# Kernel tuning notes

Hardware: AMD Instinct MI355X
Metric: run time of the kernel (lower is better)

The kernel has to match this reference:

```python
import jax, jax.numpy as jnp
import numpy as np

N, L, D_H, D_X = 512, 64, 256, 64
Q, N_TYP, N_TOK, N_MEM = 8192, 16, 32000, 262144
N_SEG = N * L


def setup_inputs() -> dict:
    key = jax.random.key(0)
    ks = jax.random.split(key, 16)
    inp = {}
    inp['h_grp'] = jax.random.normal(ks[0], (N, L, D_H), jnp.float32)
    inp['tok_emb'] = jax.random.normal(ks[1], (N_TOK, D_X), jnp.float32) * 0.02
    inp['Wq'] = jax.random.normal(ks[2], (D_H, 2 * D_H), jnp.float32) / np.sqrt(2 * D_H)
    inp['bq'] = jnp.zeros((D_H,), jnp.float32)
    inp['Wk'] = jax.random.normal(ks[3], (D_H, D_H), jnp.float32) / np.sqrt(D_H)
    inp['bk'] = jnp.zeros((D_H,), jnp.float32)
    inp['Wrel'] = jax.random.normal(ks[4], (N_TYP, 2 * D_H + D_X), jnp.float32) / np.sqrt(2 * D_H + D_X)
    inp['brel'] = jnp.zeros((N_TYP,), jnp.float32)
    inp['mem'] = jax.random.randint(ks[5], (N_MEM,), 0, N_TOK, jnp.int32)
    inp['grp'] = jax.random.randint(ks[6], (N_MEM,), 0, N_SEG, jnp.int32)
    inp['pos2grp'] = jax.random.randint(ks[7], (N, L), 0, N_SEG, jnp.int32)
    msk = jax.random.randint(ks[8], (N, L, 1), 0, 2, jnp.int32)
    inp['msk'] = msk.at[:, 0, :].set(1)  # ensure every group has a valid slot
    inp['idx'] = jnp.sort(jax.random.randint(ks[9], (Q,), 0, N, jnp.int32))
    inp['src'] = jax.random.randint(ks[10], (Q,), 0, L, jnp.int32)
    inp['dst'] = jax.random.randint(ks[11], (Q,), 0, L, jnp.int32)
    inp['typ'] = jax.random.randint(ks[12], (Q, N_TYP), 0, 2, jnp.int32)
    return inp


def reference(h_grp, tok_emb, Wq, bq, Wk, bk, Wrel, brel,
              mem, grp, pos2grp, msk, idx, src, dst, typ):
    n, l, d_h = h_grp.shape
    # x_grp = scatter_sum(tok_embedding(mem), grp, 0)[pos2grp]  -> (n, l, d_x)
    x_sum = jax.ops.segment_sum(tok_emb[mem], grp, num_segments=N_SEG)
    x_grp = x_sum[pos2grp]
    # q = cat([h_grp[idx, src], h_grp[idx, dst]], -1)  -> (Q, 2*d_h)
    q_in = jnp.concatenate([h_grp[idx, src], h_grp[idx, dst]], axis=-1)
    # attention(): per-query attention over its group's l positions
    qp = q_in @ Wq.T + bq                                # (Q, d_h)
    kp = h_grp @ Wk.T + bk                               # (n, l, d_h)
    s = jnp.einsum('qld,qd->ql', kp[idx], qp) / jnp.sqrt(jnp.float32(d_h))
    valid = msk[idx, :, 0].astype(bool)                  # (Q, l)
    s = jnp.where(valid, s, -jnp.inf)
    a = jax.nn.softmax(s, axis=1)                        # (Q, l)
    attn = jnp.einsum('ql,qld->qd', a, x_grp[idx])       # (Q, d_x)
    # rel head
    logit = jnp.concatenate([q_in, attn], axis=-1) @ Wrel.T + brel  # (Q, n_typ)
    # metrics
    gt = logit > 0
    eq = gt == (typ > 0)
    acc = eq.astype(jnp.float32).mean()
    em = jax.ops.segment_min(jnp.all(eq, axis=1).astype(jnp.int32), idx, num_segments=n)
    emr = em.astype(jnp.float32).mean()
    return logit, acc, emr, em
```

## Files before the change

kernel.cpp:

```cpp
#include <hip/hip_runtime.h>
#include <math.h>

#define N_    512
#define L_    64
#define DH    256
#define DX    64
#define Q_    8192
#define NTYP  16
#define NMEM  262144
#define NSEG  32768

typedef short bf16x8 __attribute__((ext_vector_type(8)));
typedef float f32x4  __attribute__((ext_vector_type(4)));

__device__ inline ushort f2bf(float x) {
    unsigned u = __float_as_uint(x);
    unsigned r = u + 0x7FFFu + ((u >> 16) & 1u);
    return (ushort)(r >> 16);
}

__global__ void k_init(int* __restrict__ em, int* __restrict__ eqcnt) {
    int t = blockIdx.x * blockDim.x + threadIdx.x;
    if (t < N_) em[t] = 0x7fffffff;
    if (t == 0) *eqcnt = 0;
}

__global__ __launch_bounds__(256) void k_hist(const int* __restrict__ grp,
                                              int* __restrict__ counts) {
    int e = blockIdx.x * 256 + threadIdx.x;
    atomicAdd(&counts[grp[e]], 1);
}

__global__ __launch_bounds__(1024) void k_scan(const int* __restrict__ counts,
                                               int* __restrict__ offsets,
                                               int* __restrict__ cursor) {
    __shared__ int ls[1024];
    int t = threadIdx.x;
    int c[32];
    int base = t * 32;
    int s = 0;
#pragma unroll
    for (int i = 0; i < 32; i++) { c[i] = counts[base + i]; s += c[i]; }
    ls[t] = s;
    __syncthreads();
    for (int off = 1; off < 1024; off <<= 1) {
        int v = (t >= off) ? ls[t - off] : 0;
        __syncthreads();
        ls[t] += v;
        __syncthreads();
    }
    int excl = (t == 0) ? 0 : ls[t - 1];
#pragma unroll
    for (int i = 0; i < 32; i++) {
        offsets[base + i] = excl;
        cursor[base + i] = excl;
        excl += c[i];
    }
}

__global__ __launch_bounds__(256) void k_bucket(const int* __restrict__ grp,
                                                const int* __restrict__ mem,
                                                int* __restrict__ cursor,
                                                int* __restrict__ sorted_mem) {
    int e = blockIdx.x * 256 + threadIdx.x;
    int g = grp[e];
    int pos = atomicAdd(&cursor[g], 1);
    sorted_mem[pos] = mem[e];
}

__global__ __launch_bounds__(256) void k_gsum(const float* __restrict__ tok,
                                              const int* __restrict__ sorted_mem,
                                              const int* __restrict__ offsets,
                                              const int* __restrict__ counts,
                                              float* __restrict__ xsum) {
    int g = blockIdx.x * 4 + (threadIdx.x >> 6);
    int lane = threadIdx.x & 63;
    int beg = offsets[g], cnt = counts[g];
    float acc = 0.f;
    for (int j = 0; j < cnt; j++) {
        int m = sorted_mem[beg + j];
        acc += tok[(size_t)m * 64 + lane];
    }
    xsum[(size_t)g * 64 + lane] = acc;
}

__global__ __launch_bounds__(256) void k_wcvt(const float* __restrict__ Wq,
                                              const float* __restrict__ Wk,
                                              const float* __restrict__ Wrel,
                                              ushort* __restrict__ Wqbf,
                                              ushort* __restrict__ WkTbf,
                                              ushort* __restrict__ Wrelbf) {
    int i = blockIdx.x * 256 + threadIdx.x;
    if (i < 131072) Wqbf[i] = f2bf(Wq[i]);
    if (i < 65536) {
        int kk = i >> 8, e = i & 255;
        WkTbf[e * 256 + kk] = f2bf(Wk[i]);
    }
    if (i < 9216) Wrelbf[i] = f2bf(Wrel[i]);
}

__global__ __launch_bounds__(256) void k_qin(const float* __restrict__ h,
                                             const int* __restrict__ idx,
                                             const int* __restrict__ src,
                                             const int* __restrict__ dst,
                                             ushort* __restrict__ qin) {
    int q = blockIdx.x * 2 + (threadIdx.x >> 7);
    int t = threadIdx.x & 127;
    int r = idx[q];
    int pos = (t < 64) ? src[q] : dst[q];
    float4 v = *(const float4*)(h + ((size_t)r * 64 + pos) * 256 + (t & 63) * 4);
    ushort4 o = { f2bf(v.x), f2bf(v.y), f2bf(v.z), f2bf(v.w) };
    *(ushort4*)(qin + (size_t)q * 512 + t * 4) = o;
}

__global__ __launch_bounds__(256) void k_gqp(const ushort* __restrict__ qin,
                                             const ushort* __restrict__ Wqbf,
                                             const float* __restrict__ bq,
                                             ushort* __restrict__ qp_bf) {
    int w = threadIdx.x >> 6, l = threadIdx.x & 63;
    int qb = (blockIdx.x >> 2) * 64 + (w >> 1) * 32;
    int db = (blockIdx.x & 3) * 64 + (w & 1) * 32;
    int lr = l & 15, lk = (l >> 4) * 8;
    f32x4 a00 = {0.f,0.f,0.f,0.f}, a01 = a00, a10 = a00, a11 = a00;
#pragma unroll 4
    for (int k0 = 0; k0 < 512; k0 += 32) {
        bf16x8 fa0 = *(const bf16x8*)(qin + (size_t)(qb + lr) * 512 + k0 + lk);
        bf16x8 fa1 = *(const bf16x8*)(qin + (size_t)(qb + 16 + lr) * 512 + k0 + lk);
        bf16x8 fb0 = *(const bf16x8*)(Wqbf + (size_t)(db + lr) * 512 + k0 + lk);
        bf16x8 fb1 = *(const bf16x8*)(Wqbf + (size_t)(db + 16 + lr) * 512 + k0 + lk);
        a00 = __builtin_amdgcn_mfma_f32_16x16x32_bf16(fa0, fb0, a00, 0, 0, 0);
        a01 = __builtin_amdgcn_mfma_f32_16x16x32_bf16(fa0, fb1, a01, 0, 0, 0);
        a10 = __builtin_amdgcn_mfma_f32_16x16x32_bf16(fa1, fb0, a10, 0, 0, 0);
        a11 = __builtin_amdgcn_mfma_f32_16x16x32_bf16(fa1, fb1, a11, 0, 0, 0);
    }
    int ocol = l & 15;
    float b0 = bq[db + ocol], b1 = bq[db + 16 + ocol];
#pragma unroll
    for (int r = 0; r < 4; r++) {
        int row = (l >> 4) * 4 + r;
        qp_bf[(size_t)(qb + row) * 256 + db + ocol]           = f2bf(a00[r] + b0);
        qp_bf[(size_t)(qb + row) * 256 + db + 16 + ocol]      = f2bf(a01[r] + b1);
        qp_bf[(size_t)(qb + 16 + row) * 256 + db + ocol]      = f2bf(a10[r] + b0);
        qp_bf[(size_t)(qb + 16 + row) * 256 + db + 16 + ocol] = f2bf(a11[r] + b1);
    }
}

__global__ __launch_bounds__(256) void k_gqk(const ushort* __restrict__ qp_bf,
                                             const ushort* __restrict__ WkTbf,
                                             float* __restrict__ qk) {
    int w = threadIdx.x >> 6, l = threadIdx.x & 63;
    int qb = (blockIdx.x >> 2) * 64 + (w >> 1) * 32;
    int eb = (blockIdx.x & 3) * 64 + (w & 1) * 32;
    int lr = l & 15, lk = (l >> 4) * 8;
    f32x4 a00 = {0.f,0.f,0.f,0.f}, a01 = a00, a10 = a00, a11 = a00;
#pragma unroll 4
    for (int k0 = 0; k0 < 256; k0 += 32) {
        bf16x8 fa0 = *(const bf16x8*)(qp_bf + (size_t)(qb + lr) * 256 + k0 + lk);
        bf16x8 fa1 = *(const bf16x8*)(qp_bf + (size_t)(qb + 16 + lr) * 256 + k0 + lk);
        bf16x8 fb0 = *(const bf16x8*)(WkTbf + (size_t)(eb + lr) * 256 + k0 + lk);
        bf16x8 fb1 = *(const bf16x8*)(WkTbf + (size_t)(eb + 16 + lr) * 256 + k0 + lk);
        a00 = __builtin_amdgcn_mfma_f32_16x16x32_bf16(fa0, fb0, a00, 0, 0, 0);
        a01 = __builtin_amdgcn_mfma_f32_16x16x32_bf16(fa0, fb1, a01, 0, 0, 0);
        a10 = __builtin_amdgcn_mfma_f32_16x16x32_bf16(fa1, fb0, a10, 0, 0, 0);
        a11 = __builtin_amdgcn_mfma_f32_16x16x32_bf16(fa1, fb1, a11, 0, 0, 0);
    }
    int ocol = l & 15;
#pragma unroll
    for (int r = 0; r < 4; r++) {
        int row = (l >> 4) * 4 + r;
        qk[(size_t)(qb + row) * 256 + eb + ocol]           = a00[r];
        qk[(size_t)(qb + row) * 256 + eb + 16 + ocol]      = a01[r];
        qk[(size_t)(qb + 16 + row) * 256 + eb + ocol]      = a10[r];
        qk[(size_t)(qb + 16 + row) * 256 + eb + 16 + ocol] = a11[r];
    }
}

__global__ __launch_bounds__(256) void k_htr(const float* __restrict__ h,
                                             float4* __restrict__ hT4) {
    __shared__ float hsT[256][65];
    int row = blockIdx.x;
    int t = threadIdx.x;
    const float4* h4 = (const float4*)(h + (size_t)row * 64 * 256);
    for (int i = t; i < 4096; i += 256) {
        int l = i >> 6, d4 = i & 63;
        float4 v = h4[i];
        hsT[d4 * 4 + 0][l] = v.x; hsT[d4 * 4 + 1][l] = v.y;
        hsT[d4 * 4 + 2][l] = v.z; hsT[d4 * 4 + 3][l] = v.w;
    }
    __syncthreads();
    float4* o4 = hT4 + (size_t)row * 4096;
    for (int i = t; i < 4096; i += 256) {
        int j4 = i >> 6, l = i & 63;
        float4 o = { hsT[4 * j4 + 0][l], hsT[4 * j4 + 1][l],
                     hsT[4 * j4 + 2][l], hsT[4 * j4 + 3][l] };
        o4[i] = o;
    }
}

__global__ __launch_bounds__(256) void k_attn4(const float4* __restrict__ hT4,
                                               const float* __restrict__ qk,
                                               const float* __restrict__ xsum,
                                               const int* __restrict__ pos2grp,
                                               const int* __restrict__ msk,
                                               const int* __restrict__ idx,
                                               ushort* __restrict__ attn_bf) {
    int wid  = threadIdx.x >> 6;
    int lane = threadIdx.x & 63;
    int bid = ((blockIdx.x & 7) << 8) | (blockIdx.x >> 3);
    int q = bid * 4 + wid;
    int row = idx[q];

    const float4* hT  = hT4 + (size_t)row * 4096;
    const float4* qk4 = (const float4*)(qk + (size_t)q * 256);
    float p = 0.f;
#pragma unroll 8
    for (int j4 = 0; j4 < 64; j4++) {
        float4 hv = hT[j4 * 64 + lane];
        float4 qv = qk4[j4];
        p = fmaf(hv.x, qv.x, fmaf(hv.y, qv.y,
            fmaf(hv.z, qv.z, fmaf(hv.w, qv.w, p))));
    }
    int v = msk[row * 64 + lane];
    float s = v ? p * 0.0625f : -INFINITY;

    float m = s;
#pragma unroll
    for (int off = 32; off; off >>= 1) m = fmaxf(m, __shfl_xor(m, off));
    float e = expf(s - m);
    float sum = e;
#pragma unroll
    for (int off = 32; off; off >>= 1) sum += __shfl_xor(sum, off);
    float a = e / sum;

    int g_l = pos2grp[row * 64 + lane];
    float acc = 0.f;
#pragma unroll 8
    for (int l = 0; l < 64; l++) {
        float al = __shfl(a, l);
        int g = __shfl(g_l, l);
        acc = fmaf(al, xsum[(size_t)g * 64 + lane], acc);
    }
    attn_bf[(size_t)q * 64 + lane] = f2bf(acc);
}

__global__ __launch_bounds__(256) void k_logit4(const ushort* __restrict__ qin,
                                                const ushort* __restrict__ attn_bf,
                                                const ushort* __restrict__ Wrelbf,
                                                const float* __restrict__ brel,
                                                const int* __restrict__ idx,
                                                const int* __restrict__ typ,
                                                float* __restrict__ out,
                                                int* __restrict__ em,
                                                int* __restrict__ eqcnt) {
    __shared__ int cnt;
    int w = threadIdx.x >> 6, l = threadIdx.x & 63;
    int qb = blockIdx.x * 64 + w * 16;
    int lr = l & 15, lk = (l >> 4) * 8;
    if (threadIdx.x == 0) cnt = 0;
    __syncthreads();

    f32x4 acc = {0.f, 0.f, 0.f, 0.f};
    const ushort* wrow = Wrelbf + lr * 576;
#pragma unroll 4
    for (int k0 = 0; k0 < 512; k0 += 32) {
        bf16x8 fa = *(const bf16x8*)(qin + (size_t)(qb + lr) * 512 + k0 + lk);
        bf16x8 fb = *(const bf16x8*)(wrow + k0 + lk);
        acc = __builtin_amdgcn_mfma_f32_16x16x32_bf16(fa, fb, acc, 0, 0, 0);
    }
#pragma unroll
    for (int k0 = 0; k0 < 64; k0 += 32) {
        bf16x8 fa = *(const bf16x8*)(attn_bf + (size_t)(qb + lr) * 64 + k0 + lk);
        bf16x8 fb = *(const bf16x8*)(wrow + 512 + k0 + lk);
        acc = __builtin_amdgcn_mfma_f32_16x16x32_bf16(fa, fb, acc, 0, 0, 0);
    }

    float b = brel[lr];
    int localcnt = 0;
#pragma unroll
    for (int r = 0; r < 4; r++) {
        int q = qb + (l >> 4) * 4 + r;
        float val = acc[r] + b;
        out[(size_t)q * 16 + lr] = val;
        int eq = ((val > 0.f) == (typ[q * 16 + lr] > 0)) ? 1 : 0;
        unsigned long long mask = __ballot(eq);
        if (lr == 0) {
            unsigned bits = (unsigned)((mask >> ((l >> 4) * 16)) & 0xFFFFull);
            localcnt += __popc(bits);
            int all = (bits == 0xFFFFu) ? 1 : 0;
            atomicMin(&em[idx[q]], all);
        }
    }
    if (lr == 0) atomicAdd(&cnt, localcnt);
    __syncthreads();
    if (threadIdx.x == 0) atomicAdd(eqcnt, cnt);
}

__global__ void k_fin(const int* __restrict__ em, const int* __restrict__ eqcnt,
                      float* __restrict__ out) {
    __shared__ float ssum[512];
    int t = threadIdx.x;
    int v = em[t];
    out[131074 + t] = (float)v;
    ssum[t] = (float)v;
    __syncthreads();
    for (int s = 256; s; s >>= 1) {
        if (t < s) ssum[t] += ssum[t + s];
        __syncthreads();
    }
    if (t == 0) {
        out[131073] = ssum[0] / 512.0f;
        out[131072] = (float)(*eqcnt) / (float)(Q_ * NTYP);
    }
}

extern "C" void kernel_launch(void* const* d_in, const int* in_sizes, int n_in,
                              void* d_out, int out_size, void* d_ws, size_t ws_size,
                              hipStream_t stream) {
    const float* h    = (const float*)d_in[0];
    const float* tok  = (const float*)d_in[1];
    const float* Wq   = (const float*)d_in[2];
    const float* bq   = (const float*)d_in[3];
    const float* Wk   = (const float*)d_in[4];
    const float* Wrel = (const float*)d_in[6];
    const float* brel = (const float*)d_in[7];
    const int* mem     = (const int*)d_in[8];
    const int* grp     = (const int*)d_in[9];
    const int* pos2grp = (const int*)d_in[10];
    const int* msk     = (const int*)d_in[11];
    const int* idx     = (const int*)d_in[12];
    const int* src     = (const int*)d_in[13];
    const int* dst     = (const int*)d_in[14];
    const int* typ     = (const int*)d_in[15];
    float* out = (float*)d_out;

    char* ws = (char*)d_ws;
    float* xsum    = (float*)ws;
    float* qk      = (float*)(ws + (size_t)( 8 << 20));
    ushort* qin    = (ushort*)(ws + (size_t)(16 << 20));
    ushort* qp_bf  = (ushort*)(ws + (size_t)(24 << 20));
    ushort* attn_bf= (ushort*)(ws + (size_t)(24 << 20));
    float4* hT4    = (float4*)(ws + (size_t)(28 << 20));
    int* counts     = (int*)(ws + (size_t)(60 << 20));
    int* offsets    = (int*)(ws + (size_t)(60 << 20) + (128 << 10));
    int* cursor     = (int*)(ws + (size_t)(60 << 20) + (256 << 10));
    int* sorted_mem = (int*)(ws + (size_t)(60 << 20) + (384 << 10));
    int* em         = (int*)(ws + (size_t)(61 << 20) + (512 << 10));
    int* eqcnt      = (int*)(ws + (size_t)(61 << 20) + (516 << 10));
    ushort* Wqbf    = (ushort*)(ws + (size_t)(61 << 20) + (520 << 10));
    ushort* WkTbf   = (ushort*)(ws + (size_t)(61 << 20) + (776 << 10));
    ushort* Wrelbf  = (ushort*)(ws + (size_t)(61 << 20) + (904 << 10));

    k_init<<<1, 512, 0, stream>>>(em, eqcnt);
    hipMemsetAsync(counts, 0, (size_t)NSEG * 4, stream);
    k_hist<<<NMEM / 256, 256, 0, stream>>>(grp, counts);
    k_scan<<<1, 1024, 0, stream>>>(counts, offsets, cursor);
    k_bucket<<<NMEM / 256, 256, 0, stream>>>(grp, mem, cursor, sorted_mem);
    k_gsum<<<NSEG / 4, 256, 0, stream>>>(tok, sorted_mem, offsets, counts, xsum);
    k_wcvt<<<512, 256, 0, stream>>>(Wq, Wk, Wrel, Wqbf, WkTbf, Wrelbf);
    k_qin<<<Q_ / 2, 256, 0, stream>>>(h, idx, src, dst, qin);
    k_gqp<<<(Q_ / 64) * 4, 256, 0, stream>>>(qin, Wqbf, bq, qp_bf);
    k_gqk<<<(Q_ / 64) * 4, 256, 0, stream>>>(qp_bf, WkTbf, qk);
    k_htr<<<N_, 256, 0, stream>>>(h, hT4);
    k_attn4<<<Q_ / 4, 256, 0, stream>>>(hT4, qk, xsum, pos2grp, msk, idx, attn_bf);
    k_logit4<<<Q_ / 64, 256, 0, stream>>>(qin, attn_bf, Wrelbf, brel, idx, typ, out, em, eqcnt);
    k_fin<<<1, 512, 0, stream>>>(em, eqcnt, out);
}
```

Baseline: 274.5 us.

## Fuse transpose into per-group MFMA attention kernel using sorted idx ranges

Replaces the h-transpose kernel and the per-query scalar attention kernel with one kernel per group row. Each block binary-searches the sorted idx for its query range, stages h and the gathered x_grp into shared memory as bf16, and computes scores and the attention-weighted sum with bf16 MFMA. qk is now written as bf16 instead of fp32. This removes one launch and the hT round trip, and reuses each group's h and x across all of its queries. In exchange, scores, probabilities and x lose precision, and load balance depends on how many queries land in each group.

```diff
diff --git a/kernel.cpp b/kernel.cpp
--- a/kernel.cpp
+++ b/kernel.cpp
@@ -147,7 +147,7 @@
 
 __global__ __launch_bounds__(256) void k_gqk(const ushort* __restrict__ qp_bf,
                                              const ushort* __restrict__ WkTbf,
-                                             float* __restrict__ qk) {
+                                             ushort* __restrict__ qk_bf) {
     int w = threadIdx.x >> 6, l = threadIdx.x & 63;
     int qb = (blockIdx.x >> 2) * 64 + (w >> 1) * 32;
     int eb = (blockIdx.x & 3) * 64 + (w & 1) * 32;
@@ -168,79 +168,139 @@
 #pragma unroll
     for (int r = 0; r < 4; r++) {
         int row = (l >> 4) * 4 + r;
-        qk[(size_t)(qb + row) * 256 + eb + ocol]           = a00[r];
-        qk[(size_t)(qb + row) * 256 + eb + 16 + ocol]      = a01[r];
-        qk[(size_t)(qb + 16 + row) * 256 + eb + ocol]      = a10[r];
-        qk[(size_t)(qb + 16 + row) * 256 + eb + 16 + ocol] = a11[r];
-    }
-}
-
-__global__ __launch_bounds__(256) void k_htr(const float* __restrict__ h,
-                                             float4* __restrict__ hT4) {
-    __shared__ float hsT[256][65];
-    int row = blockIdx.x;
-    int t = threadIdx.x;
-    const float4* h4 = (const float4*)(h + (size_t)row * 64 * 256);
-    for (int i = t; i < 4096; i += 256) {
-        int l = i >> 6, d4 = i & 63;
-        float4 v = h4[i];
-        hsT[d4 * 4 + 0][l] = v.x; hsT[d4 * 4 + 1][l] = v.y;
-        hsT[d4 * 4 + 2][l] = v.z; hsT[d4 * 4 + 3][l] = v.w;
-    }
-    __syncthreads();
-    float4* o4 = hT4 + (size_t)row * 4096;
-    for (int i = t; i < 4096; i += 256) {
-        int j4 = i >> 6, l = i & 63;
-        float4 o = { hsT[4 * j4 + 0][l], hsT[4 * j4 + 1][l],
-                     hsT[4 * j4 + 2][l], hsT[4 * j4 + 3][l] };
-        o4[i] = o;
-    }
-}
-
-__global__ __launch_bounds__(256) void k_attn4(const float4* __restrict__ hT4,
-                                               const float* __restrict__ qk,
+        qk_bf[(size_t)(qb + row) * 256 + eb + ocol]           = f2bf(a00[r]);
+        qk_bf[(size_t)(qb + row) * 256 + eb + 16 + ocol]      = f2bf(a01[r]);
+        qk_bf[(size_t)(qb + 16 + row) * 256 + eb + ocol]      = f2bf(a10[r]);
+        qk_bf[(size_t)(qb + 16 + row) * 256 + eb + 16 + ocol] = f2bf(a11[r]);
+    }
+}
+
+__global__ __launch_bounds__(256) void k_attn5(const float* __restrict__ h,
+                                               const ushort* __restrict__ qk_bf,
                                                const float* __restrict__ xsum,
                                                const int* __restrict__ pos2grp,
                                                const int* __restrict__ msk,
                                                const int* __restrict__ idx,
                                                ushort* __restrict__ attn_bf) {
-    int wid  = threadIdx.x >> 6;
-    int lane = threadIdx.x & 63;
-    int bid = ((blockIdx.x & 7) << 8) | (blockIdx.x >> 3);
-    int q = bid * 4 + wid;
-    int row = idx[q];
-
-    const float4* hT  = hT4 + (size_t)row * 4096;
-    const float4* qk4 = (const float4*)(qk + (size_t)q * 256);
-    float p = 0.f;
-#pragma unroll 8
-    for (int j4 = 0; j4 < 64; j4++) {
-        float4 hv = hT[j4 * 64 + lane];
-        float4 qv = qk4[j4];
-        p = fmaf(hv.x, qv.x, fmaf(hv.y, qv.y,
-            fmaf(hv.z, qv.z, fmaf(hv.w, qv.w, p))));
-    }
-    int v = msk[row * 64 + lane];
-    float s = v ? p * 0.0625f : -INFINITY;
-
-    float m = s;
-#pragma unroll
-    for (int off = 32; off; off >>= 1) m = fmaxf(m, __shfl_xor(m, off));
-    float e = expf(s - m);
-    float sum = e;
-#pragma unroll
-    for (int off = 32; off; off >>= 1) sum += __shfl_xor(sum, off);
-    float a = e / sum;
-
-    int g_l = pos2grp[row * 64 + lane];
-    float acc = 0.f;
-#pragma unroll 8
-    for (int l = 0; l < 64; l++) {
-        float al = __shfl(a, l);
-        int g = __shfl(g_l, l);
-        acc = fmaf(al, xsum[(size_t)g * 64 + lane], acc);
-    }
-    attn_bf[(size_t)q * 64 + lane] = f2bf(acc);
+    __shared__ ushort hs[64][264];
+    __shared__ ushort xgT[64][72];
+    __shared__ float  svalid[64];
+    __shared__ ushort pa[4][16][72];
+
+    int row = blockIdx.x;
+    int lo = 0, hi = Q_;
+    while (lo < hi) { int mid = (lo + hi) >> 1; if (idx[mid] < row) lo = mid + 1; else hi = mid; }
+    int qlo = lo;
+    hi = Q_;
+    while (lo < hi) { int mid = (lo + hi) >> 1; if (idx[mid] <= row) lo = mid + 1; else hi = mid; }
+    int qhi = lo;
+    if (qlo == qhi) return;
+
+    int t = threadIdx.x;
+    {
+        const float4* h4 = (const float4*)(h + (size_t)row * 16384);
+        for (int i = t; i < 4096; i += 256) {
+            int l = i >> 6, d4 = i & 63;
+            float4 v = h4[i];
+            ushort4 o = { f2bf(v.x), f2bf(v.y), f2bf(v.z), f2bf(v.w) };
+            *(ushort4*)(&hs[l][d4 * 4]) = o;
+        }
+    }
+    {
+        int pos = t & 63, part = t >> 6;
+        int g = pos2grp[row * 64 + pos];
+#pragma unroll
+        for (int m = 0; m < 4; m++) {
+            float4 v = *(const float4*)(xsum + (size_t)g * 64 + part * 16 + m * 4);
+            int d = part * 16 + m * 4;
+            xgT[d + 0][pos] = f2bf(v.x);
+            xgT[d + 1][pos] = f2bf(v.y);
+            xgT[d + 2][pos] = f2bf(v.z);
+            xgT[d + 3][pos] = f2bf(v.w);
+        }
+    }
+    if (t < 64) svalid[t] = msk[row * 64 + t] ? 0.f : -INFINITY;
+    __syncthreads();
+
+    int w = t >> 6, l = t & 63;
+    int lr = l & 15, lk = (l >> 4) * 8;
+
+    for (int c0 = qlo + w * 16; c0 < qhi; c0 += 64) {
+        int qa = c0 + lr; if (qa >= qhi) qa = qhi - 1;
+
+        f32x4 sacc[4];
+        sacc[0] = (f32x4){0.f,0.f,0.f,0.f}; sacc[1] = sacc[0];
+        sacc[2] = sacc[0]; sacc[3] = sacc[0];
+#pragma unroll
+        for (int k0 = 0; k0 < 256; k0 += 32) {
+            bf16x8 fa = *(const bf16x8*)(qk_bf + (size_t)qa * 256 + k0 + lk);
+            bf16x8 fb0 = *(const bf16x8*)(&hs[ 0 + lr][k0 + lk]);
+            bf16x8 fb1 = *(const bf16x8*)(&hs[16 + lr][k0 + lk]);
+            bf16x8 fb2 = *(const bf16x8*)(&hs[32 + lr][k0 + lk]);
+            bf16x8 fb3 = *(const bf16x8*)(&hs[48 + lr][k0 + lk]);
+            sacc[0] = __builtin_amdgcn_mfma_f32_16x16x32_bf16(fa, fb0, sacc[0], 0, 0, 0);
+            sacc[1] = __builtin_amdgcn_mfma_f32_16x16x32_bf16(fa, fb1, sacc[1], 0, 0, 0);
+            sacc[2] = __builtin_amdgcn_mfma_f32_16x16x32_bf16(fa, fb2, sacc[2], 0, 0, 0);
+            sacc[3] = __builtin_amdgcn_mfma_f32_16x16x32_bf16(fa, fb3, sacc[3], 0, 0, 0);
+        }
+
+        float s[4][4];
+#pragma unroll
+        for (int pt = 0; pt < 4; pt++) {
+            float vmask = svalid[pt * 16 + lr];
+#pragma unroll
+            for (int r = 0; r < 4; r++) s[pt][r] = sacc[pt][r] * 0.0625f + vmask;
+        }
+#pragma unroll
+        for (int r = 0; r < 4; r++) {
+            float m = fmaxf(fmaxf(s[0][r], s[1][r]), fmaxf(s[2][r], s[3][r]));
+            m = fmaxf(m, __shfl_xor(m, 1));
+            m = fmaxf(m, __shfl_xor(m, 2));
+            m = fmaxf(m, __shfl_xor(m, 4));
+            m = fmaxf(m, __shfl_xor(m, 8));
+#pragma unroll
+            for (int pt = 0; pt < 4; pt++) s[pt][r] = expf(s[pt][r] - m);
+            float ss = ((s[0][r] + s[1][r]) + (s[2][r] + s[3][r]));
+            ss += __shfl_xor(ss, 1);
+            ss += __shfl_xor(ss, 2);
+            ss += __shfl_xor(ss, 4);
+            ss += __shfl_xor(ss, 8);
+            float inv = 1.f / ss;
+#pragma unroll
+            for (int pt = 0; pt < 4; pt++) s[pt][r] *= inv;
+        }
+
+#pragma unroll
+        for (int pt = 0; pt < 4; pt++)
+#pragma unroll
+            for (int r = 0; r < 4; r++)
+                pa[w][(l >> 4) * 4 + r][pt * 16 + lr] = f2bf(s[pt][r]);
+
+        f32x4 oacc[4];
+        oacc[0] = (f32x4){0.f,0.f,0.f,0.f}; oacc[1] = oacc[0];
+        oacc[2] = oacc[0]; oacc[3] = oacc[0];
+#pragma unroll
+        for (int k0 = 0; k0 < 64; k0 += 32) {
+            bf16x8 fa2 = *(const bf16x8*)(&pa[w][lr][k0 + lk]);
+            bf16x8 fb0 = *(const bf16x8*)(&xgT[ 0 + lr][k0 + lk]);
+            bf16x8 fb1 = *(const bf16x8*)(&xgT[16 + lr][k0 + lk]);
+            bf16x8 fb2 = *(const bf16x8*)(&xgT[32 + lr][k0 + lk]);
+            bf16x8 fb3 = *(const bf16x8*)(&xgT[48 + lr][k0 + lk]);
+            oacc[0] = __builtin_amdgcn_mfma_f32_16x16x32_bf16(fa2, fb0, oacc[0], 0, 0, 0);
+            oacc[1] = __builtin_amdgcn_mfma_f32_16x16x32_bf16(fa2, fb1, oacc[1], 0, 0, 0);
+            oacc[2] = __builtin_amdgcn_mfma_f32_16x16x32_bf16(fa2, fb2, oacc[2], 0, 0, 0);
+            oacc[3] = __builtin_amdgcn_mfma_f32_16x16x32_bf16(fa2, fb3, oacc[3], 0, 0, 0);
+        }
+#pragma unroll
+        for (int r = 0; r < 4; r++) {
+            int q = c0 + (l >> 4) * 4 + r;
+            if (q < qhi) {
+#pragma unroll
+                for (int dt = 0; dt < 4; dt++)
+                    attn_bf[(size_t)q * 64 + dt * 16 + lr] = f2bf(oacc[dt][r]);
+            }
+        }
+    }
 }
 
 __global__ __launch_bounds__(256) void k_logit4(const ushort* __restrict__ qin,
@@ -335,11 +395,10 @@
 
     char* ws = (char*)d_ws;
     float* xsum    = (float*)ws;
-    float* qk      = (float*)(ws + (size_t)( 8 << 20));
+    ushort* qk_bf  = (ushort*)(ws + (size_t)( 8 << 20));
     ushort* qin    = (ushort*)(ws + (size_t)(16 << 20));
     ushort* qp_bf  = (ushort*)(ws + (size_t)(24 << 20));
     ushort* attn_bf= (ushort*)(ws + (size_t)(24 << 20));
-    float4* hT4    = (float4*)(ws + (size_t)(28 << 20));
     int* counts     = (int*)(ws + (size_t)(60 << 20));
     int* offsets    = (int*)(ws + (size_t)(60 << 20) + (128 << 10));
     int* cursor     = (int*)(ws + (size_t)(60 << 20) + (256 << 10));
@@ -359,9 +418,8 @@
     k_wcvt<<<512, 256, 0, stream>>>(Wq, Wk, Wrel, Wqbf, WkTbf, Wrelbf);
     k_qin<<<Q_ / 2, 256, 0, stream>>>(h, idx, src, dst, qin);
     k_gqp<<<(Q_ / 64) * 4, 256, 0, stream>>>(qin, Wqbf, bq, qp_bf);
-    k_gqk<<<(Q_ / 64) * 4, 256, 0, stream>>>(qp_bf, WkTbf, qk);
-    k_htr<<<N_, 256, 0, stream>>>(h, hT4);
-    k_attn4<<<Q_ / 4, 256, 0, stream>>>(hT4, qk, xsum, pos2grp, msk, idx, attn_bf);
+    k_gqk<<<(Q_ / 64) * 4, 256, 0, stream>>>(qp_bf, WkTbf, qk_bf);
+    k_attn5<<<N_, 256, 0, stream>>>(h, qk_bf, xsum, pos2grp, msk, idx, attn_bf);
     k_logit4<<<Q_ / 64, 256, 0, stream>>>(qin, attn_bf, Wrelbf, brel, idx, typ, out, em, eqcnt);
     k_fin<<<1, 512, 0, stream>>>(em, eqcnt, out);
 }
```

Result: faster. 239.0 us (-12.9%).
